# Optimization experiments

Hardware: AMD Instinct MI355X
Metric: run time of the kernel (lower is better)

## Reference

```python
import jax, jax.numpy as jnp
import numpy as np

C = 4          # num_components
B = 2          # true batch
HEADS = 24
DIM_HEAD = 64
D = HEADS * DIM_HEAD      # 1536, attn.out_dim == query dim
CROSS = 2048              # encoder hidden dim
S = 2048                  # latent sequence length
E = 77                    # encoder sequence length
PAD = 77                  # pad_length (must equal E for the broadcast in the original code)


def setup_inputs() -> dict:
    key = jax.random.key(0)
    ks = jax.random.split(key, 12)
    w = 0.02
    return {
        "hidden_states": jax.random.normal(ks[0], (B * C, S, D), jnp.float32),
        "encoder_hidden_states": jax.random.normal(ks[1], (B * C, E, CROSS), jnp.float32),
        "Wq": jax.random.normal(ks[2], (D, D), jnp.float32) * w,
        "bq": jax.random.normal(ks[3], (D,), jnp.float32) * w,
        "Wk": jax.random.normal(ks[4], (D, CROSS), jnp.float32) * w,
        "bk": jax.random.normal(ks[5], (D,), jnp.float32) * w,
        "Wv": jax.random.normal(ks[6], (D, CROSS), jnp.float32) * w,
        "bv": jax.random.normal(ks[7], (D,), jnp.float32) * w,
        "Wo": jax.random.normal(ks[8], (D, D), jnp.float32) * w,
        "bo": jax.random.normal(ks[9], (D,), jnp.float32) * w,
        "pad_length": PAD,
    }


def reference(hidden_states, encoder_hidden_states, Wq, bq, Wk, bk, Wv, bv, Wo, bo, pad_length):
    BC, S_, D_ = hidden_states.shape
    E_ = encoder_hidden_states.shape[1]
    Bsz = BC // C
    scale = 1.0 / np.sqrt(DIM_HEAD)

    # projections (torch nn.Linear: x @ W.T + b)
    q = hidden_states @ Wq.T + bq                      # [BC, S, D]
    k = encoder_hidden_states @ Wk.T + bk              # [BC, E, D]
    v = encoder_hidden_states @ Wv.T + bv              # [BC, E, D]
    # pad branch: to_k/to_v applied to zeros -> just the bias, broadcast over pad tokens
    k_pad = jnp.broadcast_to(bk, (BC, pad_length, D_))  # [BC, PAD, D]
    v_pad = jnp.broadcast_to(bv, (BC, pad_length, D_))
    v = jnp.concatenate([v, v_pad], axis=1)            # [BC, E+PAD, D]

    # split heads
    qh = q.reshape(BC, S_, HEADS, DIM_HEAD)
    kh = k.reshape(BC, E_, HEADS, DIM_HEAD)
    kph = k_pad.reshape(BC, pad_length, HEADS, DIM_HEAD)
    vh = v.reshape(BC, E_ + pad_length, HEADS, DIM_HEAD)

    # scores: [BC, H, S, E] and [BC, H, S, PAD]
    scores = jnp.einsum("bihd,bjhd->bhij", qh, kh) * scale
    scores_pad = jnp.einsum("bihd,bjhd->bhij", qh, kph) * scale

    # component-wise softmax: view as [C, B, H, S, *], softmax over component axis 0
    scores = scores.reshape(C, Bsz, HEADS, S_, E_)
    scores_pad = scores_pad.reshape(C, Bsz, HEADS, S_, pad_length)
    w_main = jax.nn.softmax(scores, axis=0)
    w_pad = jax.nn.softmax(scores_pad, axis=0) * (C / pad_length) * (1.0 - w_main)

    w_main = w_main.reshape(BC, HEADS, S_, E_)
    w_pad = w_pad.reshape(BC, HEADS, S_, pad_length)
    weights = jnp.concatenate([w_main, w_pad], axis=-1)  # [BC, H, S, E+PAD]

    # attention @ V -> merge heads
    out = jnp.einsum("bhij,bjhd->bihd", weights, vh).reshape(BC, S_, D_)
    out = out @ Wo.T + bo   # to_out[0]; dropout is identity in eval
    return out
```

## Files before the change

### kernel.cpp

```cpp
#include <hip/hip_runtime.h>
#include <hip/hip_bf16.h>


typedef __attribute__((ext_vector_type(8))) short short8;
typedef __attribute__((ext_vector_type(4))) float f32x4;
typedef __attribute__((ext_vector_type(4))) _Float16 half4;

#define DEV __device__ __forceinline__

DEV ushort f2bf(float x) {
  __hip_bfloat16 h = __float2bfloat16(x);
  return *reinterpret_cast<ushort*>(&h);
}


__global__ __launch_bounds__(256) void cvt_all(const float* __restrict__ hs, ushort* __restrict__ hs_bf,
                                               const float* __restrict__ Wq, ushort* __restrict__ Wq_bf,
                                               const float* __restrict__ Wk, ushort* __restrict__ Wk_bf,
                                               const float* __restrict__ Wv, ushort* __restrict__ Wv_bf,
                                               const float* __restrict__ Wo, ushort* __restrict__ Wo_bf,
                                               const float* __restrict__ ehs, ushort* __restrict__ ehs_bf) {
  const int b0 = 6291456;
  const int b1 = b0 + 589824;
  const int b2 = b1 + 786432;
  const int b3 = b2 + 786432;
  const int b4 = b3 + 589824;
  const int total = b4 + 327680;
  int idx = blockIdx.x * blockDim.x + threadIdx.x;
  int stride = gridDim.x * blockDim.x;
  for (int q = idx; q < total; q += stride) {
    const float* in; ushort* out; int qq;
    bool zero = false;
    if (q < b0)      { in = hs;  out = hs_bf;  qq = q; }
    else if (q < b1) { in = Wq;  out = Wq_bf;  qq = q - b0; }
    else if (q < b2) { in = Wk;  out = Wk_bf;  qq = q - b1; }
    else if (q < b3) { in = Wv;  out = Wv_bf;  qq = q - b2; }
    else if (q < b4) { in = Wo;  out = Wo_bf;  qq = q - b3; }
    else {
      qq = q - b4;
      int r = qq >> 9;
      in = ehs; out = ehs_bf;
      zero = (r >= 616);
    }
    ushort4 o;
    if (!zero) {
      float4 f = reinterpret_cast<const float4*>(in)[qq];
      o.x = f2bf(f.x); o.y = f2bf(f.y); o.z = f2bf(f.z); o.w = f2bf(f.w);
    } else {
      o.x = 0; o.y = 0; o.z = 0; o.w = 0;
    }
    reinterpret_cast<ushort4*>(out)[qq] = o;
  }
}


template <typename OutT>
DEV void gemm_body(const ushort* __restrict__ A, const ushort* __restrict__ B,
                   const float* __restrict__ bias, OutT* __restrict__ C,
                   int M, int N, int K) {
  __shared__ __align__(16) ushort lds[32768];
  const int tid = threadIdx.x;
  const int lane = tid & 63;
  const int wid = tid >> 6;
  const int wr = wid >> 1, wc = wid & 1;
  const long m0 = (long)blockIdx.x * 128;
  const long n0 = (long)blockIdx.y * 128;
  const int ll = lane & 15, g = lane >> 4;
  const int swz = ll & 7;

  const int srow = wid * 8 + (lane >> 3);
  const int scol = ((lane & 7) ^ (lane >> 3)) * 8;
  const ushort* pa = A + (m0 + srow) * (long)K + scol;
  const ushort* pb = B + (n0 + srow) * (long)K + scol;
  const long qstep = 32 * (long)K;

  f32x4 acc[4][4] = {};

#define STAGE(tt, bsel)                                                                    \
  do {                                                                                     \
    const long kt_ = (long)(tt) * 64;                                                      \
    const int ab_ = (bsel) * 32768 + wid * 1024;                                           \
    _Pragma("unroll") for (int q = 0; q < 4; ++q)                                          \
        __builtin_amdgcn_global_load_lds(                                                  \
            (const __attribute__((address_space(1))) void*)(pa + kt_ + q * qstep),         \
            (__attribute__((address_space(3))) void*)((char*)lds + ab_ + q * 4096),        \
            16, 0, 0);                                                                     \
    _Pragma("unroll") for (int q = 0; q < 4; ++q)                                          \
        __builtin_amdgcn_global_load_lds(                                                  \
            (const __attribute__((address_space(1))) void*)(pb + kt_ + q * qstep),         \
            (__attribute__((address_space(3))) void*)((char*)lds + ab_ + 16384 + q * 4096),\
            16, 0, 0);                                                                     \
  } while (0)

  const int nt = K >> 6;
  STAGE(0, 0);
  STAGE(1, 1);
  asm volatile("s_waitcnt vmcnt(8)" ::: "memory");
  __builtin_amdgcn_s_barrier();

  for (int t = 0; t < nt; ++t) {
    const int buf = t & 1;
    const char* abase = (const char*)lds + buf * 32768;
    const char* bbase = abase + 16384;
    short8 af[4][2], bfr[4][2];
#pragma unroll
    for (int m = 0; m < 4; ++m)
#pragma unroll
      for (int ks = 0; ks < 2; ++ks)
        af[m][ks] = *reinterpret_cast<const short8*>(
            abase + (wr * 64 + m * 16 + ll) * 128 + (((ks * 4 + g) ^ swz) * 16));
#pragma unroll
    for (int n = 0; n < 4; ++n)
#pragma unroll
      for (int ks = 0; ks < 2; ++ks)
        bfr[n][ks] = *reinterpret_cast<const short8*>(
            bbase + (wc * 64 + n * 16 + ll) * 128 + (((ks * 4 + g) ^ swz) * 16));
    asm volatile("s_waitcnt lgkmcnt(0)" ::: "memory");
    __builtin_amdgcn_s_barrier();

    if (t < nt - 2) {
      STAGE(t + 2, buf);
      asm volatile("s_waitcnt vmcnt(8)" ::: "memory");
    } else if (t == nt - 2) {
      asm volatile("s_waitcnt vmcnt(0)" ::: "memory");
    }
    __builtin_amdgcn_sched_barrier(0);
    __builtin_amdgcn_s_setprio(1);
#pragma unroll
    for (int ks = 0; ks < 2; ++ks)
#pragma unroll
      for (int m = 0; m < 4; ++m)
#pragma unroll
        for (int n = 0; n < 4; ++n)
          acc[m][n] =
              __builtin_amdgcn_mfma_f32_16x16x32_bf16(af[m][ks], bfr[n][ks], acc[m][n], 0, 0, 0);
    __builtin_amdgcn_s_setprio(0);
    __builtin_amdgcn_s_barrier();
  }
#undef STAGE

#pragma unroll
  for (int m = 0; m < 4; ++m) {
#pragma unroll
    for (int n = 0; n < 4; ++n) {
      const int row = wr * 64 + m * 16 + g * 4;
      const int col = wc * 64 + n * 16 + ll;
      const float bias_v = bias[n0 + col];
#pragma unroll
      for (int r = 0; r < 4; ++r) {
        float val = acc[m][n][r] + bias_v;
        long off = (m0 + row + r) * (long)N + n0 + col;
        if constexpr (sizeof(OutT) == 2) {
          C[off] = (OutT)f2bf(val);
        } else {
          C[off] = val;
        }
      }
    }
  }
}

template <typename OutT>
__global__ __launch_bounds__(256) void gemm_p(const ushort* __restrict__ A,
                                              const ushort* __restrict__ B,
                                              const float* __restrict__ bias,
                                              OutT* __restrict__ C, int M, int N, int K) {
  gemm_body<OutT>(A, B, bias, C, M, N, K);
}

__global__ __launch_bounds__(256) void gemm_p_kv(const ushort* __restrict__ A,
                                                 const ushort* __restrict__ Bk,
                                                 const float* __restrict__ bk, float* Ck,
                                                 const ushort* __restrict__ Bv,
                                                 const float* __restrict__ bv, float* Cv,
                                                 int M, int N, int K) {
  if (blockIdx.z == 0)
    gemm_body<float>(A, Bk, bk, Ck, M, N, K);
  else
    gemm_body<float>(A, Bv, bv, Cv, M, N, K);
}


__global__ __launch_bounds__(256) void prep_kv(const float* __restrict__ k_f,
                                               const float* __restrict__ v_f,
                                               const float* __restrict__ bk,
                                               const float* __restrict__ bv,
                                               ushort* __restrict__ kimg,
                                               ushort* __restrict__ vimg) {
  __shared__ _Float16 vl[80][68];
  const int c = blockIdx.x, h = blockIdx.y, bb = blockIdx.z;
  const int tid = threadIdx.x;
  const long ibase = ((long)(bb * 24 + h)) * 20480 + c * 5120;

  for (int rr = tid; rr < 640; rr += 256) {
    int j = rr >> 3, t = rr & 7;
    short8 v = {};
    const float* src = nullptr;
    if (j < 77)
      src = k_f + ((long)((c * 2 + bb) * 77 + j)) * 1536 + h * 64 + t * 8;
    else if (j == 77)
      src = bk + h * 64 + t * 8;
    if (src) {
      float4 f0 = reinterpret_cast<const float4*>(src)[0];
      float4 f1 = reinterpret_cast<const float4*>(src)[1];
      v[0] = f2bf(f0.x); v[1] = f2bf(f0.y); v[2] = f2bf(f0.z); v[3] = f2bf(f0.w);
      v[4] = f2bf(f1.x); v[5] = f2bf(f1.y); v[6] = f2bf(f1.z); v[7] = f2bf(f1.w);
    }
    *reinterpret_cast<short8*>(kimg + ibase + j * 64 + (t ^ (j & 7)) * 8) = v;
  }
  for (int rr = tid; rr < 640; rr += 256) {
    int j = rr >> 3, t = rr & 7;
    half4 lo = {}, hi = {};
    const float* src = nullptr;
    if (j < 77)
      src = v_f + ((long)((c * 2 + bb) * 77 + j)) * 1536 + h * 64 + t * 8;
    else if (j == 77)
      src = bv + h * 64 + t * 8;
    if (src) {
      float4 f0 = reinterpret_cast<const float4*>(src)[0];
      float4 f1 = reinterpret_cast<const float4*>(src)[1];
      lo[0] = (_Float16)f0.x; lo[1] = (_Float16)f0.y; lo[2] = (_Float16)f0.z; lo[3] = (_Float16)f0.w;
      hi[0] = (_Float16)f1.x; hi[1] = (_Float16)f1.y; hi[2] = (_Float16)f1.z; hi[3] = (_Float16)f1.w;
    }
    *reinterpret_cast<half4*>(&vl[j][t * 8]) = lo;
    *reinterpret_cast<half4*>(&vl[j][t * 8 + 4]) = hi;
  }
  __syncthreads();
  const int d = tid & 63, jg = tid >> 6;
  ushort* vrow = vimg + ibase + d * 80;
  const int x = (d >> 2) & 3;
#pragma unroll
  for (int b = 0; b < 5; ++b) {
    int jb = jg * 5 + b;
    half4 hv;
#pragma unroll
    for (int e = 0; e < 4; ++e) hv[e] = vl[jb * 4 + e][d];
    *reinterpret_cast<half4*>(vrow + ((jb ^ x) << 2)) = hv;
  }
}


__global__ __launch_bounds__(256) void attn_v4(const ushort* __restrict__ qg,
                                               const ushort* __restrict__ kimg,
                                               const ushort* __restrict__ vimg,
                                               ushort* __restrict__ ao) {
  __shared__ __align__(16) ushort vt[20480];
  const int tid = threadIdx.x;
  const int lane = tid & 63;
  const int w = tid >> 6;
  const int h = blockIdx.y, bb = blockIdx.z;
  const int i0 = blockIdx.x * 64;
  const long ib = ((long)(bb * 24 + h)) * 20480;

#pragma unroll
  for (int p = 0; p < 10; ++p) {
    int is = p * 4 + w;
    __builtin_amdgcn_global_load_lds(
        (const __attribute__((address_space(1))) void*)(vimg + ib + is * 512 + lane * 8),
        (__attribute__((address_space(3))) void*)((char*)vt + is * 1024), 16, 0, 0);
  }

  const int ll = lane & 15, g = lane >> 4;

  f32x4 s[4][5];
#pragma unroll
  for (int c = 0; c < 4; ++c)
#pragma unroll
    for (int m = 0; m < 5; ++m) s[c][m] = (f32x4){0.f, 0.f, 0.f, 0.f};

#pragma unroll
  for (int c = 0; c < 4; ++c) {
    const ushort* qbase =
        qg + ((long)((c * 2 + bb) * 2048 + i0 + w * 16 + ll)) * 1536 + h * 64 + g * 8;
    short8 qf0 = *reinterpret_cast<const short8*>(qbase);
    short8 qf1 = *reinterpret_cast<const short8*>(qbase + 32);
    const ushort* kbase = kimg + ib + c * 5120;
#pragma unroll
    for (int m = 0; m < 5; ++m) {
      const ushort* rb = kbase + (m * 16 + ll) * 64;
      short8 a0 = *reinterpret_cast<const short8*>(rb + (g ^ (ll & 7)) * 8);
      short8 a1 = *reinterpret_cast<const short8*>(rb + ((4 + g) ^ (ll & 7)) * 8);
      s[c][m] = __builtin_amdgcn_mfma_f32_16x16x32_bf16(a0, qf0, s[c][m], 0, 0, 0);
      s[c][m] = __builtin_amdgcn_mfma_f32_16x16x32_bf16(a1, qf1, s[c][m], 0, 0, 0);
    }
  }

  const float scale = 0.125f;
  float wsum0 = 0.f, wsum1 = 0.f, wsum2 = 0.f, wsum3 = 0.f;
#pragma unroll
  for (int m = 0; m < 5; ++m) {
#pragma unroll
    for (int e = 0; e < 4; ++e) {
      float x0 = s[0][m][e] * scale, x1 = s[1][m][e] * scale;
      float x2 = s[2][m][e] * scale, x3 = s[3][m][e] * scale;
      float mx = fmaxf(fmaxf(x0, x1), fmaxf(x2, x3));
      float e0 = __expf(x0 - mx), e1 = __expf(x1 - mx);
      float e2 = __expf(x2 - mx), e3 = __expf(x3 - mx);
      float inv = __fdividef(1.f, e0 + e1 + e2 + e3);
      float w0 = e0 * inv, w1 = e1 * inv, w2 = e2 * inv, w3 = e3 * inv;
      int jj = m * 16 + g * 4 + e;
      float msk = (jj < 77) ? 1.f : 0.f;
      wsum0 += w0 * msk; wsum1 += w1 * msk; wsum2 += w2 * msk; wsum3 += w3 * msk;
      s[0][m][e] = w0; s[1][m][e] = w1; s[2][m][e] = w2; s[3][m][e] = w3;
    }
  }
  wsum0 += __shfl_xor(wsum0, 16); wsum0 += __shfl_xor(wsum0, 32);
  wsum1 += __shfl_xor(wsum1, 16); wsum1 += __shfl_xor(wsum1, 32);
  wsum2 += __shfl_xor(wsum2, 16); wsum2 += __shfl_xor(wsum2, 32);
  wsum3 += __shfl_xor(wsum3, 16); wsum3 += __shfl_xor(wsum3, 32);

  const bool g3 = (g == 3);
  {
    float wsum[4] = {wsum0, wsum1, wsum2, wsum3};
#pragma unroll
    for (int c = 0; c < 4; ++c) {
      float w77 = s[c][4][1];
      float pwv = w77 * (4.0f / 77.0f) * (77.0f - wsum[c]);
      s[c][4][1] = g3 ? pwv : w77;
      s[c][4][2] = g3 ? 0.f : s[c][4][2];
      s[c][4][3] = g3 ? 0.f : s[c][4][3];
    }
  }

  half4 wf[4][5];
#pragma unroll
  for (int c = 0; c < 4; ++c)
#pragma unroll
    for (int m = 0; m < 5; ++m) {
      half4 hv;
      hv[0] = (_Float16)s[c][m][0];
      hv[1] = (_Float16)s[c][m][1];
      hv[2] = (_Float16)s[c][m][2];
      hv[3] = (_Float16)s[c][m][3];
      wf[c][m] = hv;
    }

  __syncthreads();

  f32x4 o[4][4];
#pragma unroll
  for (int c = 0; c < 4; ++c)
#pragma unroll
    for (int n = 0; n < 4; ++n) o[c][n] = (f32x4){0.f, 0.f, 0.f, 0.f};

#pragma unroll
  for (int c = 0; c < 4; ++c)
#pragma unroll
    for (int m = 0; m < 5; ++m)
#pragma unroll
      for (int n = 0; n < 4; ++n) {
        const int dd = n * 16 + ll;
        const int jb = (m * 4 + g) ^ ((dd >> 2) & 3);
        half4 vf = *reinterpret_cast<const half4*>(
            reinterpret_cast<const _Float16*>(vt) + c * 5120 + dd * 80 + (jb << 2));
        o[c][n] = __builtin_amdgcn_mfma_f32_16x16x16f16(wf[c][m], vf, o[c][n], 0, 0, 0);
      }

#pragma unroll
  for (int c = 0; c < 4; ++c)
#pragma unroll
    for (int n = 0; n < 4; ++n)
#pragma unroll
      for (int r = 0; r < 4; ++r) {
        long row = (long)((c * 2 + bb) * 2048 + i0 + w * 16 + g * 4 + r);
        ao[row * 1536 + h * 64 + n * 16 + ll] = f2bf(o[c][n][r]);
      }
}


extern "C" void kernel_launch(void* const* d_in, const int* in_sizes, int n_in,
                              void* d_out, int out_size, void* d_ws, size_t ws_size,
                              hipStream_t stream) {
  (void)in_sizes; (void)n_in; (void)out_size; (void)ws_size;
  const float* hs  = (const float*)d_in[0];
  const float* ehs = (const float*)d_in[1];
  const float* Wq  = (const float*)d_in[2];
  const float* bq  = (const float*)d_in[3];
  const float* Wk  = (const float*)d_in[4];
  const float* bk  = (const float*)d_in[5];
  const float* Wv  = (const float*)d_in[6];
  const float* bv  = (const float*)d_in[7];
  const float* Wo  = (const float*)d_in[8];
  const float* bo  = (const float*)d_in[9];
  float* out = (float*)d_out;

  char* ws = (char*)d_ws;
  size_t off = 0;
  auto alloc = [&](size_t bytes) {
    char* p = ws + off;
    off += (bytes + 255) & ~(size_t)255;
    return p;
  };
  ushort* hs_bf  = (ushort*)alloc(16384UL * 1536 * 2);
  ushort* ehs_bf = (ushort*)alloc(640UL * 2048 * 2);
  ushort* Wq_bf  = (ushort*)alloc(1536UL * 1536 * 2);
  ushort* Wk_bf  = (ushort*)alloc(1536UL * 2048 * 2);
  ushort* Wv_bf  = (ushort*)alloc(1536UL * 2048 * 2);
  ushort* Wo_bf  = (ushort*)alloc(1536UL * 1536 * 2);
  ushort* q_bf   = (ushort*)alloc(16384UL * 1536 * 2);
  float*  k_f    = (float*)alloc(640UL * 1536 * 4);
  float*  v_f    = (float*)alloc(640UL * 1536 * 4);
  ushort* ao_bf  = (ushort*)alloc(16384UL * 1536 * 2);
  ushort* kimg   = (ushort*)alloc(48UL * 20480 * 2);
  ushort* vimg   = (ushort*)alloc(48UL * 20480 * 2);

  dim3 b256(256);
  cvt_all<<<4096, b256, 0, stream>>>(hs, hs_bf, Wq, Wq_bf, Wk, Wk_bf, Wv, Wv_bf,
                                     Wo, Wo_bf, ehs, ehs_bf);

  gemm_p_kv<<<dim3(5, 12, 2), b256, 0, stream>>>(ehs_bf, Wk_bf, bk, k_f, Wv_bf, bv, v_f,
                                                 640, 1536, 2048);
  prep_kv<<<dim3(4, 24, 2), b256, 0, stream>>>(k_f, v_f, bk, bv, kimg, vimg);
  gemm_p<ushort><<<dim3(128, 12), b256, 0, stream>>>(hs_bf, Wq_bf, bq, q_bf, 16384, 1536, 1536);
  attn_v4<<<dim3(32, 24, 2), b256, 0, stream>>>(q_bf, kimg, vimg, ao_bf);
  gemm_p<float><<<dim3(128, 12), b256, 0, stream>>>(ao_bf, Wo_bf, bo, out, 16384, 1536, 1536);
}
```

Measured before the change: 268.2 us.

## Fuse fp32-to-bf16 conversion of hidden states into Q projection GEMM

Removes the standalone conversion of hidden_states to bf16 and adds a Q GEMM kernel that loads fp32 A tiles into registers, converts them to bf16, and writes them swizzled into LDS, double-buffered alongside direct-to-LDS B loads. This avoids writing and re-reading a large bf16 intermediate. The trade-off is that A is now read as fp32 by every N-tile block, and the GEMM carries extra register and conversion work in its main loop.

```diff
diff --git a/kernel.cpp b/kernel.cpp
--- a/kernel.cpp
+++ b/kernel.cpp
@@ -14,14 +14,12 @@
 }
 
 
-__global__ __launch_bounds__(256) void cvt_all(const float* __restrict__ hs, ushort* __restrict__ hs_bf,
-                                               const float* __restrict__ Wq, ushort* __restrict__ Wq_bf,
+__global__ __launch_bounds__(256) void cvt_all(const float* __restrict__ Wq, ushort* __restrict__ Wq_bf,
                                                const float* __restrict__ Wk, ushort* __restrict__ Wk_bf,
                                                const float* __restrict__ Wv, ushort* __restrict__ Wv_bf,
                                                const float* __restrict__ Wo, ushort* __restrict__ Wo_bf,
                                                const float* __restrict__ ehs, ushort* __restrict__ ehs_bf) {
-  const int b0 = 6291456;
-  const int b1 = b0 + 589824;
+  const int b1 = 589824;
   const int b2 = b1 + 786432;
   const int b3 = b2 + 786432;
   const int b4 = b3 + 589824;
@@ -31,8 +29,7 @@
   for (int q = idx; q < total; q += stride) {
     const float* in; ushort* out; int qq;
     bool zero = false;
-    if (q < b0)      { in = hs;  out = hs_bf;  qq = q; }
-    else if (q < b1) { in = Wq;  out = Wq_bf;  qq = q - b0; }
+    if (q < b1)      { in = Wq;  out = Wq_bf;  qq = q; }
     else if (q < b2) { in = Wk;  out = Wk_bf;  qq = q - b1; }
     else if (q < b3) { in = Wv;  out = Wv_bf;  qq = q - b2; }
     else if (q < b4) { in = Wo;  out = Wo_bf;  qq = q - b3; }
@@ -181,6 +178,143 @@
 }
 
 
+__global__ __launch_bounds__(256) void gemm_qf(const float* __restrict__ A,
+                                               const ushort* __restrict__ B,
+                                               const float* __restrict__ bias,
+                                               ushort* __restrict__ C, int M, int N, int K) {
+  __shared__ __align__(16) ushort lds[32768];
+  const int tid = threadIdx.x;
+  const int lane = tid & 63;
+  const int wid = tid >> 6;
+  const int wr = wid >> 1, wc = wid & 1;
+  const long m0 = (long)blockIdx.x * 128;
+  const long n0 = (long)blockIdx.y * 128;
+  const int ll = lane & 15, g = lane >> 4;
+  const int swz = ll & 7;
+
+  const int srow = wid * 8 + (lane >> 3);
+  const int scol = ((lane & 7) ^ (lane >> 3)) * 8;
+  const ushort* pb = B + (n0 + srow) * (long)K + scol;
+  const long qstep = 32 * (long)K;
+
+  const int arow = tid >> 3;
+  const int acol = (tid & 7) * 8;
+  const int awz = ((tid & 7) ^ ((tid >> 3) & 7)) * 16;
+  const float* paf = A + (m0 + arow) * (long)K + acol;
+  const long arstep = 32 * (long)K;
+
+  f32x4 acc[4][4] = {};
+  float4 R0[8], R1[8];
+
+#define STAGEB(tt, bsel)                                                                   \
+  do {                                                                                     \
+    const long kt_ = (long)(tt) * 64;                                                      \
+    const int bb_ = (bsel) * 32768 + 16384 + wid * 1024;                                   \
+    _Pragma("unroll") for (int q = 0; q < 4; ++q)                                          \
+        __builtin_amdgcn_global_load_lds(                                                  \
+            (const __attribute__((address_space(1))) void*)(pb + kt_ + q * qstep),         \
+            (__attribute__((address_space(3))) void*)((char*)lds + bb_ + q * 4096),        \
+            16, 0, 0);                                                                     \
+  } while (0)
+
+#define ALOAD(tt, R)                                                                       \
+  do {                                                                                     \
+    const long kt_ = (long)(tt) * 64;                                                      \
+    _Pragma("unroll") for (int q = 0; q < 4; ++q) {                                        \
+      (R)[2 * q]     = *reinterpret_cast<const float4*>(paf + kt_ + q * arstep);           \
+      (R)[2 * q + 1] = *reinterpret_cast<const float4*>(paf + kt_ + q * arstep + 4);       \
+    }                                                                                      \
+  } while (0)
+
+#define WRITEA(R, bsel)                                                                    \
+  do {                                                                                     \
+    char* ab_ = (char*)lds + (bsel) * 32768;                                               \
+    _Pragma("unroll") for (int q = 0; q < 4; ++q) {                                        \
+      short8 v_;                                                                           \
+      v_[0] = (short)f2bf((R)[2 * q].x);  v_[1] = (short)f2bf((R)[2 * q].y);               \
+      v_[2] = (short)f2bf((R)[2 * q].z);  v_[3] = (short)f2bf((R)[2 * q].w);               \
+      v_[4] = (short)f2bf((R)[2 * q + 1].x); v_[5] = (short)f2bf((R)[2 * q + 1].y);        \
+      v_[6] = (short)f2bf((R)[2 * q + 1].z); v_[7] = (short)f2bf((R)[2 * q + 1].w);        \
+      *reinterpret_cast<short8*>(ab_ + (q * 32 + arow) * 128 + awz) = v_;                  \
+    }                                                                                      \
+  } while (0)
+
+  const int nt = K >> 6;
+  STAGEB(0, 0);
+  STAGEB(1, 1);
+  ALOAD(0, R0);
+  ALOAD(1, R1);
+  asm volatile("s_waitcnt vmcnt(8)" ::: "memory");
+  WRITEA(R0, 0);
+  asm volatile("s_waitcnt lgkmcnt(0)" ::: "memory");
+  __builtin_amdgcn_s_barrier();
+
+#define GBODY(T, RW, RL)                                                                   \
+  do {                                                                                     \
+    const int t_ = (T);                                                                    \
+    const int buf_ = t_ & 1;                                                               \
+    const char* abase = (const char*)lds + buf_ * 32768;                                   \
+    const char* bbase = abase + 16384;                                                     \
+    short8 af[4][2], bfr[4][2];                                                            \
+    _Pragma("unroll") for (int m = 0; m < 4; ++m)                                          \
+      _Pragma("unroll") for (int ks = 0; ks < 2; ++ks)                                     \
+        af[m][ks] = *reinterpret_cast<const short8*>(                                      \
+            abase + (wr * 64 + m * 16 + ll) * 128 + (((ks * 4 + g) ^ swz) * 16));          \
+    _Pragma("unroll") for (int n = 0; n < 4; ++n)                                          \
+      _Pragma("unroll") for (int ks = 0; ks < 2; ++ks)                                     \
+        bfr[n][ks] = *reinterpret_cast<const short8*>(                                     \
+            bbase + (wc * 64 + n * 16 + ll) * 128 + (((ks * 4 + g) ^ swz) * 16));          \
+    asm volatile("s_waitcnt lgkmcnt(0)" ::: "memory");                                     \
+    __builtin_amdgcn_s_barrier();                                                          \
+    if (t_ < nt - 2) {                                                                     \
+      STAGEB(t_ + 2, buf_);                                                                \
+      ALOAD(t_ + 2, RL);                                                                   \
+      asm volatile("s_waitcnt vmcnt(12)" ::: "memory");                                    \
+    } else if (t_ == nt - 2) {                                                             \
+      asm volatile("s_waitcnt vmcnt(0)" ::: "memory");                                     \
+    }                                                                                      \
+    __builtin_amdgcn_sched_barrier(0);                                                     \
+    if (t_ < nt - 1) WRITEA(RW, (t_ + 1) & 1);                                             \
+    __builtin_amdgcn_sched_barrier(0);                                                     \
+    __builtin_amdgcn_s_setprio(1);                                                         \
+    _Pragma("unroll") for (int ks = 0; ks < 2; ++ks)                                       \
+      _Pragma("unroll") for (int m = 0; m < 4; ++m)                                        \
+        _Pragma("unroll") for (int n = 0; n < 4; ++n)                                      \
+          acc[m][n] =                                                                      \
+              __builtin_amdgcn_mfma_f32_16x16x32_bf16(af[m][ks], bfr[n][ks], acc[m][n],    \
+                                                      0, 0, 0);                            \
+    __builtin_amdgcn_s_setprio(0);                                                         \
+    asm volatile("s_waitcnt lgkmcnt(0)" ::: "memory");                                     \
+    __builtin_amdgcn_s_barrier();                                                          \
+  } while (0)
+
+  for (int tt = 0; tt < nt; tt += 2) {
+    GBODY(tt, R1, R0);
+    GBODY(tt + 1, R0, R1);
+  }
+#undef GBODY
+#undef WRITEA
+#undef ALOAD
+#undef STAGEB
+
+#pragma unroll
+  for (int m = 0; m < 4; ++m) {
+#pragma unroll
+    for (int n = 0; n < 4; ++n) {
+      const int row = wr * 64 + m * 16 + g * 4;
+      const int col = wc * 64 + n * 16 + ll;
+      const float bias_v = bias[n0 + col];
+#pragma unroll
+      for (int r = 0; r < 4; ++r) {
+        float val = acc[m][n][r] + bias_v;
+        long off = (m0 + row + r) * (long)N + n0 + col;
+        C[off] = (ushort)f2bf(val);
+      }
+    }
+  }
+}
+
+
 __global__ __launch_bounds__(256) void prep_kv(const float* __restrict__ k_f,
                                                const float* __restrict__ v_f,
                                                const float* __restrict__ bk,
@@ -391,7 +525,6 @@
     off += (bytes + 255) & ~(size_t)255;
     return p;
   };
-  ushort* hs_bf  = (ushort*)alloc(16384UL * 1536 * 2);
   ushort* ehs_bf = (ushort*)alloc(640UL * 2048 * 2);
   ushort* Wq_bf  = (ushort*)alloc(1536UL * 1536 * 2);
   ushort* Wk_bf  = (ushort*)alloc(1536UL * 2048 * 2);
@@ -405,13 +538,13 @@
   ushort* vimg   = (ushort*)alloc(48UL * 20480 * 2);
 
   dim3 b256(256);
-  cvt_all<<<4096, b256, 0, stream>>>(hs, hs_bf, Wq, Wq_bf, Wk, Wk_bf, Wv, Wv_bf,
+  cvt_all<<<2048, b256, 0, stream>>>(Wq, Wq_bf, Wk, Wk_bf, Wv, Wv_bf,
                                      Wo, Wo_bf, ehs, ehs_bf);
 
   gemm_p_kv<<<dim3(5, 12, 2), b256, 0, stream>>>(ehs_bf, Wk_bf, bk, k_f, Wv_bf, bv, v_f,
                                                  640, 1536, 2048);
   prep_kv<<<dim3(4, 24, 2), b256, 0, stream>>>(k_f, v_f, bk, bv, kimg, vimg);
-  gemm_p<ushort><<<dim3(128, 12), b256, 0, stream>>>(hs_bf, Wq_bf, bq, q_bf, 16384, 1536, 1536);
+  gemm_qf<<<dim3(128, 12), b256, 0, stream>>>(hs, Wq_bf, bq, q_bf, 16384, 1536, 1536);
   attn_v4<<<dim3(32, 24, 2), b256, 0, stream>>>(q_bf, kimg, vimg, ao_bf);
   gemm_p<float><<<dim3(128, 12), b256, 0, stream>>>(ao_bf, Wo_bf, bo, out, 16384, 1536, 1536);
 }
```

Measured after the change: 293.8 us. 9.5% more time.

## Replace Q and output projection GEMMs with 256x256-tile 4-stage LDS-pipelined kernel

Applied to the files above, without the earlier changes.

Adds a new GEMM kernel with 512 threads, 256x256 output tiles, and a 4-deep ring of LDS buffers filled by direct global-to-LDS loads with manual vmcnt waits. It also uses an XOR swizzle and a remapped block order for L2 locality, and raises wave priority around the MFMA section. The Q projection and the output projection now use this kernel instead of the old 256-thread gemm_p. The goal is more operand reuse per tile and better overlap of loads with MFMA work, at the cost of 128KB of dynamic LDS per block and heavy register pressure from 32 accumulators per thread, which may limit occupancy.

```diff
diff --git a/kernel.cpp b/kernel.cpp
--- a/kernel.cpp
+++ b/kernel.cpp
@@ -160,14 +160,6 @@
   }
 }
 
-template <typename OutT>
-__global__ __launch_bounds__(256) void gemm_p(const ushort* __restrict__ A,
-                                              const ushort* __restrict__ B,
-                                              const float* __restrict__ bias,
-                                              OutT* __restrict__ C, int M, int N, int K) {
-  gemm_body<OutT>(A, B, bias, C, M, N, K);
-}
-
 __global__ __launch_bounds__(256) void gemm_p_kv(const ushort* __restrict__ A,
                                                  const ushort* __restrict__ Bk,
                                                  const float* __restrict__ bk, float* Ck,
@@ -178,6 +170,109 @@
     gemm_body<float>(A, Bk, bk, Ck, M, N, K);
   else
     gemm_body<float>(A, Bv, bv, Cv, M, N, K);
+}
+
+
+template <typename OutT>
+__global__ __launch_bounds__(512, 2) void gemm4b(const ushort* __restrict__ A,
+                                                 const ushort* __restrict__ B,
+                                                 const float* __restrict__ bias,
+                                                 OutT* __restrict__ C,
+                                                 int M, int N, int K, int nnx) {
+  extern __shared__ char dl[];
+  const int tid = threadIdx.x;
+  const int lane = tid & 63;
+  const int w = tid >> 6;
+  const int wr = w >> 2, wc = w & 3;
+  const int ll = lane & 15, g = lane >> 4;
+  const int swz = ll & 3;
+
+  const int cpx = gridDim.x >> 3;
+  const int sw = (blockIdx.x & 7) * cpx + (blockIdx.x >> 3);
+  const long m0 = (long)(sw / nnx) * 256;
+  const long n0 = (long)(sw % nnx) * 256;
+
+  const int srow = tid >> 2;
+  const int scol = ((tid & 3) ^ (srow & 3)) * 8;
+  const ushort* pa = A + (m0 + srow) * (long)K + scol;
+  const ushort* pb = B + (n0 + srow) * (long)K + scol;
+  const long rstep = 128 * (long)K;
+
+  f32x4 acc[8][4] = {};
+
+#define STG(tt)                                                                            \
+  do {                                                                                     \
+    const long kt_ = (long)(tt) * 32;                                                      \
+    char* buf_ = dl + ((tt) & 3) * 32768;                                                  \
+    _Pragma("unroll") for (int q = 0; q < 2; ++q) {                                        \
+      __builtin_amdgcn_global_load_lds(                                                    \
+          (const __attribute__((address_space(1))) void*)(pa + kt_ + q * rstep),           \
+          (__attribute__((address_space(3))) void*)(buf_ + q * 8192 + tid * 16),           \
+          16, 0, 0);                                                                       \
+      __builtin_amdgcn_global_load_lds(                                                    \
+          (const __attribute__((address_space(1))) void*)(pb + kt_ + q * rstep),           \
+          (__attribute__((address_space(3))) void*)(buf_ + 16384 + q * 8192 + tid * 16),   \
+          16, 0, 0);                                                                       \
+    }                                                                                      \
+  } while (0)
+
+  const int nt = K >> 5;
+  STG(0);
+  STG(1);
+  STG(2);
+
+  for (int t = 0; t < nt; ++t) {
+    if (t < nt - 2)
+      asm volatile("s_waitcnt vmcnt(8)" ::: "memory");
+    else if (t == nt - 2)
+      asm volatile("s_waitcnt vmcnt(4)" ::: "memory");
+    else
+      asm volatile("s_waitcnt vmcnt(0)" ::: "memory");
+    __builtin_amdgcn_s_barrier();
+
+    const char* ab = dl + (t & 3) * 32768;
+    const char* bb = ab + 16384;
+    short8 af[8], bfr[4];
+#pragma unroll
+    for (int m = 0; m < 8; ++m)
+      af[m] = *reinterpret_cast<const short8*>(
+          ab + (wr * 128 + m * 16 + ll) * 64 + ((g ^ swz) * 16));
+#pragma unroll
+    for (int n = 0; n < 4; ++n)
+      bfr[n] = *reinterpret_cast<const short8*>(
+          bb + (wc * 64 + n * 16 + ll) * 64 + ((g ^ swz) * 16));
+    if (t < nt - 3) STG(t + 3);
+    asm volatile("s_waitcnt lgkmcnt(0)" ::: "memory");
+    __builtin_amdgcn_sched_barrier(0);
+    __builtin_amdgcn_s_setprio(1);
+#pragma unroll
+    for (int m = 0; m < 8; ++m)
+#pragma unroll
+      for (int n = 0; n < 4; ++n)
+        acc[m][n] = __builtin_amdgcn_mfma_f32_16x16x32_bf16(af[m], bfr[n], acc[m][n], 0, 0, 0);
+    __builtin_amdgcn_s_setprio(0);
+  }
+#undef STG
+
+#pragma unroll
+  for (int m = 0; m < 8; ++m) {
+#pragma unroll
+    for (int n = 0; n < 4; ++n) {
+      const int row = wr * 128 + m * 16 + g * 4;
+      const int col = wc * 64 + n * 16 + ll;
+      const float bias_v = bias[n0 + col];
+#pragma unroll
+      for (int r = 0; r < 4; ++r) {
+        float val = acc[m][n][r] + bias_v;
+        long off = (m0 + row + r) * (long)N + n0 + col;
+        if constexpr (sizeof(OutT) == 2) {
+          C[off] = (OutT)f2bf(val);
+        } else {
+          C[off] = val;
+        }
+      }
+    }
+  }
 }
 
 
@@ -404,6 +499,11 @@
   ushort* kimg   = (ushort*)alloc(48UL * 20480 * 2);
   ushort* vimg   = (ushort*)alloc(48UL * 20480 * 2);
 
+  hipFuncSetAttribute(reinterpret_cast<const void*>(&gemm4b<ushort>),
+                      hipFuncAttributeMaxDynamicSharedMemorySize, 131072);
+  hipFuncSetAttribute(reinterpret_cast<const void*>(&gemm4b<float>),
+                      hipFuncAttributeMaxDynamicSharedMemorySize, 131072);
+
   dim3 b256(256);
   cvt_all<<<4096, b256, 0, stream>>>(hs, hs_bf, Wq, Wq_bf, Wk, Wk_bf, Wv, Wv_bf,
                                      Wo, Wo_bf, ehs, ehs_bf);
@@ -411,7 +511,7 @@
   gemm_p_kv<<<dim3(5, 12, 2), b256, 0, stream>>>(ehs_bf, Wk_bf, bk, k_f, Wv_bf, bv, v_f,
                                                  640, 1536, 2048);
   prep_kv<<<dim3(4, 24, 2), b256, 0, stream>>>(k_f, v_f, bk, bv, kimg, vimg);
-  gemm_p<ushort><<<dim3(128, 12), b256, 0, stream>>>(hs_bf, Wq_bf, bq, q_bf, 16384, 1536, 1536);
+  gemm4b<ushort><<<384, 512, 131072, stream>>>(hs_bf, Wq_bf, bq, q_bf, 16384, 1536, 1536, 6);
   attn_v4<<<dim3(32, 24, 2), b256, 0, stream>>>(q_bf, kimg, vimg, ao_bf);
-  gemm_p<float><<<dim3(128, 12), b256, 0, stream>>>(ao_bf, Wo_bf, bo, out, 16384, 1536, 1536);
-}
+  gemm4b<float><<<384, 512, 131072, stream>>>(ao_bf, Wo_bf, bo, out, 16384, 1536, 1536, 6);
+}
```

After: 294.3 us. 1.1x slower.
